# Kernel tuning notes

Measured on AMD Instinct MI355X. Metric: run time of the kernel, lower is better.

Reference implementation:

```python
import jax, jax.numpy as jnp
import numpy as np

WIN = 9  # local window size per spatial dim

def _boxfilter3d(x):
    k = jnp.ones((1, 1, WIN, WIN, WIN), x.dtype) / float(WIN ** 3)
    return jax.lax.conv_general_dilated(
        x, k, window_strides=(1, 1, 1), padding='SAME',
        dimension_numbers=('NCDHW', 'OIDHW', 'NCDHW'))

def setup_inputs() -> dict:
    key = jax.random.key(0)
    k1, k2 = jax.random.split(key)
    shape = (2, 1, 160, 192, 160)
    y_true = jax.random.uniform(k1, shape, dtype=jnp.float32)
    y_pred = jax.random.uniform(k2, shape, dtype=jnp.float32)
    return {"y_true": y_true, "y_pred": y_pred}

def reference(y_true, y_pred):
    Ii, Ji = y_true, y_pred
    mu1 = _boxfilter3d(Ii)
    mu2 = _boxfilter3d(Ji)
    sigma1_sq = _boxfilter3d(Ii * Ii) - mu1 * mu1
    sigma2_sq = _boxfilter3d(Ji * Ji) - mu2 * mu2
    sigma12 = _boxfilter3d(Ii * Ji) - mu1 * mu2
    cc = (sigma12 * sigma12) / (sigma1_sq * sigma2_sq + 1e-5)
    return -jnp.mean(cc)
```

## Files before the change

### kernel.cpp

```cpp
#include <hip/hip_runtime.h>

#define DD 160
#define HH 192
#define WW 160
#define HWs (HH * WW)
#define NTOT 9830400.0f
#define DOUT 20
#define NIT  28
#define NBLK 960

#define SDS 11
#define SDC (24 * SDS + 1)
#define SDP (5 * SDC)
#define HSS 11
#define HSC (16 * HSS + 1)
#define HSP (5 * HSC)

typedef float    v4 __attribute__((ext_vector_type(4)));
typedef _Float16 h4 __attribute__((ext_vector_type(4)));

__device__ __forceinline__ void block_sync_lds() {
    __builtin_amdgcn_s_waitcnt(0xc07f);
    __builtin_amdgcn_s_barrier();
}
__device__ __forceinline__ v4 up(h4 x) { return __builtin_convertvector(x, v4); }
__device__ __forceinline__ h4 dn(v4 x) { return __builtin_convertvector(x, h4); }

__global__ __launch_bounds__(256, 4) void kf(const float* __restrict__ I,
                                             const float* __restrict__ J,
                                             float* __restrict__ partial) {
    __shared__ h4    SDL[2 * SDP];
    __shared__ h4    HSL[2 * HSP];
    __shared__ float red[256];

    const int tid = threadIdx.x;
    const int bx = blockIdx.x, by = blockIdx.y, b = blockIdx.z;
    const int w0 = (bx % 5) * 32, h0 = (bx / 5) * 16;
    const int d0 = by * DOUT;
    const int bid = bx + 60 * (by + 8 * b);

    const int rt = tid ^ ((bx & 1) << 7);

    const bool p1 = rt < 240;
    const int r = rt / 10, g = rt % 10;
    const int gh = h0 - 4 + r, gw = w0 - 4 + g * 4;
    const bool colOK = p1 && gh >= 0 && gh < HH && gw >= 0 && gw < WW;
    const size_t colOff = (size_t)gh * WW + gw;
    const float* Ib = I + (size_t)b * DD * HWs + colOff;
    const float* Jb = J + (size_t)b * DD * HWs + colOff;
    h4* const sdw = &SDL[r * SDS + g];

    const bool p2 = rt < 100;
    const int g2 = rt % 10, ch2 = (rt / 10) % 5, hh0 = (rt / 50) * 8;
    const int sdrOff = ch2 * SDC + hh0 * SDS + g2;
    const int hswOff = ch2 * HSC + hh0 * HSS + g2;

    const bool p3 = rt >= 128;
    const int q3 = rt & 127;
    const int hh = q3 >> 3, sg = q3 & 7;
    const int hsrOff = hh * HSS + sg;

    v4 sd0 = 0.f, sd1 = 0.f, sd2 = 0.f, sd3 = 0.f, sd4 = 0.f;
    h4 fI[9], fJ[9];
#pragma unroll
    for (int u = 0; u < 9; ++u) { fI[u] = (h4)(_Float16)0; fJ[u] = (h4)(_Float16)0; }
    v4 pLI = 0.f, pLJ = 0.f;
    float acc = 0.f;
    const float inv = 1.0f / 729.0f;

    {
        const int si = d0 - 4;
        if (colOK && si >= 0) {
            pLI = *(const v4*)(Ib + (size_t)si * HWs);
            pLJ = *(const v4*)(Jb + (size_t)si * HWs);
        }
    }

    for (int tb = 0; tb < 36; tb += 9) {
#pragma unroll
        for (int u = 0; u < 9; ++u) {
            const int t = tb + u;
            if (t < NIT + 2) {
                if (t < NIT && p1) {
                    h4 cI = dn(pLI), cJ = dn(pLJ);
                    v4 aI = up(cI), aJ = up(cJ);
                    v4 dI = aI, dJv = aJ;
                    v4 dII = aI * aI, dJJ = aJ * aJ, dIJ = aI * aJ;
                    if (t >= 9) {
                        v4 bI = up(fI[u]), bJ = up(fJ[u]);
                        dI -= bI; dJv -= bJ;
                        dII -= bI * bI; dJJ -= bJ * bJ; dIJ -= bI * bJ;
                    }
                    fI[u] = cI; fJ[u] = cJ;
                    sd0 += dI; sd1 += dJv; sd2 += dII; sd3 += dJJ; sd4 += dIJ;
                    h4* const sdq = sdw + (t & 1) * SDP;
                    sdq[0]       = dn(sd0);
                    sdq[SDC]     = dn(sd1);
                    sdq[2 * SDC] = dn(sd2);
                    sdq[3 * SDC] = dn(sd3);
                    sdq[4 * SDC] = dn(sd4);
                    pLI = 0.f; pLJ = 0.f;
                    const int sn = d0 - 3 + t;
                    if (t + 1 < NIT && colOK && sn >= 0 && sn < DD) {
                        pLI = *(const v4*)(Ib + (size_t)sn * HWs);
                        pLJ = *(const v4*)(Jb + (size_t)sn * HWs);
                    }
                }

                if (t >= 1 && t <= NIT && p2) {
                    const int par = (t - 1) & 1;
                    const h4* const sdr = &SDL[par * SDP + sdrOff];
                    h4* const hsw = &HSL[par * HSP + hswOff];
                    h4 s = sdr[0];
#pragma unroll
                    for (int k = 1; k < 9; ++k) s += sdr[k * SDS];
                    hsw[0] = s;
#pragma unroll
                    for (int j = 1; j < 8; ++j) {
                        s += sdr[(j + 8) * SDS] - sdr[(j - 1) * SDS];
                        hsw[j * HSS] = s;
                    }
                }

                if (t >= 10 && p3) {
                    const h4* const hsr = &HSL[(t & 1) * HSP + hsrOff];
                    float w[5][4];
#pragma unroll
                    for (int c = 0; c < 5; ++c) {
                        v4 fa = up(hsr[c * HSC]);
                        v4 fb = up(hsr[c * HSC + 1]);
                        v4 fc = up(hsr[c * HSC + 2]);
                        float s = fa[0] + fa[1] + fa[2] + fa[3] +
                                  fb[0] + fb[1] + fb[2] + fb[3] + fc[0];
                        w[c][0] = s;
                        s += fc[1] - fa[0]; w[c][1] = s;
                        s += fc[2] - fa[1]; w[c][2] = s;
                        s += fc[3] - fa[2]; w[c][3] = s;
                    }
#pragma unroll
                    for (int e = 0; e < 4; ++e) {
                        float mu1 = w[0][e] * inv, mu2 = w[1][e] * inv;
                        float g1  = fmaf(-mu1, mu1, w[2][e] * inv);
                        float g2v = fmaf(-mu2, mu2, w[3][e] * inv);
                        float g12 = fmaf(-mu1, mu2, w[4][e] * inv);
                        acc += __fdividef(g12 * g12, fmaf(g1, g2v, 1e-5f));
                    }
                }

                block_sync_lds();
            }
        }
    }

    red[tid] = acc;
    __syncthreads();
    if (tid < 128) red[tid] += red[tid + 128];
    __syncthreads();
    if (tid < 64) {
        float a = red[tid] + red[tid + 64];
#pragma unroll
        for (int off = 32; off > 0; off >>= 1) a += __shfl_down(a, off);
        if (tid == 0) partial[bid] = a;
    }
}

__global__ void k3_final(const float* __restrict__ partial,
                         float* __restrict__ out) {
    __shared__ float r[1024];
    const int i = threadIdx.x;
    r[i] = (i < NBLK) ? partial[i] : 0.f;
    __syncthreads();
    for (int off = 512; off > 0; off >>= 1) {
        if (i < off) r[i] += r[i + off];
        __syncthreads();
    }
    if (i == 0) out[0] = -r[0] * (1.0f / NTOT);
}

extern "C" void kernel_launch(void* const* d_in, const int* in_sizes, int n_in,
                              void* d_out, int out_size, void* d_ws, size_t ws_size,
                              hipStream_t stream) {
    (void)in_sizes; (void)n_in; (void)out_size; (void)ws_size;
    const float* I = (const float*)d_in[0];
    const float* J = (const float*)d_in[1];
    float* out     = (float*)d_out;
    float* partial = (float*)d_ws;

    dim3 grid(60, 8, 2);
    kf<<<grid, 256, 0, stream>>>(I, J, partial);
    k3_final<<<1, 1024, 0, stream>>>(partial, out);
}
```

Baseline: 151.5 us.

## Interleave channel layout in LDS, double-prefetch loads, and reuse D-sum reads

Rearranges the D-sum LDS buffer so that each column's five channels are stored together, which lets four channels go out as two 16-byte stores instead of five 8-byte stores. Global loads are prefetched two depth slices ahead, alternating between two register buffers, to hide more load latency. The ring buffer becomes 10 entries so the loop unrolls evenly by 10. The H-pass keeps its first seven loaded values in registers instead of reading them from LDS again, and float-to-half conversion now uses packed round-toward-zero cvt_pkrtz. This cuts LDS instruction count and load stalls, at the cost of more registers and slightly different rounding.

```diff
diff --git a/kernel.cpp b/kernel.cpp
--- a/kernel.cpp
+++ b/kernel.cpp
@@ -9,28 +9,33 @@
 #define NIT  28
 #define NBLK 960
 
-#define SDS 11
-#define SDC (24 * SDS + 1)
-#define SDP (5 * SDC)
-#define HSS 11
-#define HSC (16 * HSS + 1)
-#define HSP (5 * HSC)
+#define SDRS 62
+#define SDP  1492
+#define HSRS 10
+#define HSC  162
+#define HSP  810
 
 typedef float    v4 __attribute__((ext_vector_type(4)));
 typedef _Float16 h4 __attribute__((ext_vector_type(4)));
+typedef _Float16 h2 __attribute__((ext_vector_type(2)));
+typedef _Float16 h8 __attribute__((ext_vector_type(8)));
 
 __device__ __forceinline__ void block_sync_lds() {
     __builtin_amdgcn_s_waitcnt(0xc07f);
     __builtin_amdgcn_s_barrier();
 }
 __device__ __forceinline__ v4 up(h4 x) { return __builtin_convertvector(x, v4); }
-__device__ __forceinline__ h4 dn(v4 x) { return __builtin_convertvector(x, h4); }
+__device__ __forceinline__ h4 dnp(v4 x) {
+    h2 a = __builtin_bit_cast(h2, __builtin_amdgcn_cvt_pkrtz(x[0], x[1]));
+    h2 b = __builtin_bit_cast(h2, __builtin_amdgcn_cvt_pkrtz(x[2], x[3]));
+    return __builtin_shufflevector(a, b, 0, 1, 2, 3);
+}
 
 __global__ __launch_bounds__(256, 4) void kf(const float* __restrict__ I,
                                              const float* __restrict__ J,
                                              float* __restrict__ partial) {
-    __shared__ h4    SDL[2 * SDP];
-    __shared__ h4    HSL[2 * HSP];
+    __shared__ __align__(16) h4 SDL[2 * SDP];
+    __shared__ __align__(16) h4 HSL[2 * HSP];
     __shared__ float red[256];
 
     const int tid = threadIdx.x;
@@ -48,107 +53,123 @@
     const size_t colOff = (size_t)gh * WW + gw;
     const float* Ib = I + (size_t)b * DD * HWs + colOff;
     const float* Jb = J + (size_t)b * DD * HWs + colOff;
-    h4* const sdw = &SDL[r * SDS + g];
+    const int sdwOff = r * SDRS + (r >> 3) * 2 + 6 * g;
 
     const bool p2 = rt < 100;
     const int g2 = rt % 10, ch2 = (rt / 10) % 5, hh0 = (rt / 50) * 8;
-    const int sdrOff = ch2 * SDC + hh0 * SDS + g2;
-    const int hswOff = ch2 * HSC + hh0 * HSS + g2;
+    const int sdrOff = hh0 * SDRS + (hh0 >> 3) * 2 + 6 * g2 +
+                       (ch2 == 4 ? 4 + (g2 & 1) : ch2);
+    const int hswOff = ch2 * HSC + hh0 * HSRS + g2;
 
     const bool p3 = rt >= 128;
     const int q3 = rt & 127;
     const int hh = q3 >> 3, sg = q3 & 7;
-    const int hsrOff = hh * HSS + sg;
+    const int hsrOff = hh * HSRS + sg;
 
     v4 sd0 = 0.f, sd1 = 0.f, sd2 = 0.f, sd3 = 0.f, sd4 = 0.f;
-    h4 fI[9], fJ[9];
-#pragma unroll
-    for (int u = 0; u < 9; ++u) { fI[u] = (h4)(_Float16)0; fJ[u] = (h4)(_Float16)0; }
-    v4 pLI = 0.f, pLJ = 0.f;
+    h4 fI[10], fJ[10];
+#pragma unroll
+    for (int uu = 0; uu < 10; ++uu) { fI[uu] = (h4)(_Float16)0; fJ[uu] = (h4)(_Float16)0; }
+    v4 pAI = 0.f, pAJ = 0.f, pBI = 0.f, pBJ = 0.f;
     float acc = 0.f;
     const float inv = 1.0f / 729.0f;
 
     {
-        const int si = d0 - 4;
-        if (colOK && si >= 0) {
-            pLI = *(const v4*)(Ib + (size_t)si * HWs);
-            pLJ = *(const v4*)(Jb + (size_t)si * HWs);
+        const int s0 = d0 - 4;
+        if (colOK && s0 >= 0) {
+            pAI = *(const v4*)(Ib + (size_t)s0 * HWs);
+            pAJ = *(const v4*)(Jb + (size_t)s0 * HWs);
         }
-    }
-
-    for (int tb = 0; tb < 36; tb += 9) {
-#pragma unroll
-        for (int u = 0; u < 9; ++u) {
+        const int s1 = d0 - 3;
+        if (colOK && s1 >= 0) {
+            pBI = *(const v4*)(Ib + (size_t)s1 * HWs);
+            pBJ = *(const v4*)(Jb + (size_t)s1 * HWs);
+        }
+    }
+
+    for (int tb = 0; tb < 30; tb += 10) {
+#pragma unroll
+        for (int u = 0; u < 10; ++u) {
             const int t = tb + u;
-            if (t < NIT + 2) {
-                if (t < NIT && p1) {
-                    h4 cI = dn(pLI), cJ = dn(pLJ);
-                    v4 aI = up(cI), aJ = up(cJ);
-                    v4 dI = aI, dJv = aJ;
-                    v4 dII = aI * aI, dJJ = aJ * aJ, dIJ = aI * aJ;
-                    if (t >= 9) {
-                        v4 bI = up(fI[u]), bJ = up(fJ[u]);
-                        dI -= bI; dJv -= bJ;
-                        dII -= bI * bI; dJJ -= bJ * bJ; dIJ -= bI * bJ;
-                    }
-                    fI[u] = cI; fJ[u] = cJ;
-                    sd0 += dI; sd1 += dJv; sd2 += dII; sd3 += dJJ; sd4 += dIJ;
-                    h4* const sdq = sdw + (t & 1) * SDP;
-                    sdq[0]       = dn(sd0);
-                    sdq[SDC]     = dn(sd1);
-                    sdq[2 * SDC] = dn(sd2);
-                    sdq[3 * SDC] = dn(sd3);
-                    sdq[4 * SDC] = dn(sd4);
-                    pLI = 0.f; pLJ = 0.f;
-                    const int sn = d0 - 3 + t;
-                    if (t + 1 < NIT && colOK && sn >= 0 && sn < DD) {
-                        pLI = *(const v4*)(Ib + (size_t)sn * HWs);
-                        pLJ = *(const v4*)(Jb + (size_t)sn * HWs);
-                    }
-                }
-
-                if (t >= 1 && t <= NIT && p2) {
-                    const int par = (t - 1) & 1;
-                    const h4* const sdr = &SDL[par * SDP + sdrOff];
-                    h4* const hsw = &HSL[par * HSP + hswOff];
-                    h4 s = sdr[0];
-#pragma unroll
-                    for (int k = 1; k < 9; ++k) s += sdr[k * SDS];
-                    hsw[0] = s;
-#pragma unroll
-                    for (int j = 1; j < 8; ++j) {
-                        s += sdr[(j + 8) * SDS] - sdr[(j - 1) * SDS];
-                        hsw[j * HSS] = s;
-                    }
-                }
-
-                if (t >= 10 && p3) {
-                    const h4* const hsr = &HSL[(t & 1) * HSP + hsrOff];
-                    float w[5][4];
-#pragma unroll
-                    for (int c = 0; c < 5; ++c) {
-                        v4 fa = up(hsr[c * HSC]);
-                        v4 fb = up(hsr[c * HSC + 1]);
-                        v4 fc = up(hsr[c * HSC + 2]);
-                        float s = fa[0] + fa[1] + fa[2] + fa[3] +
-                                  fb[0] + fb[1] + fb[2] + fb[3] + fc[0];
-                        w[c][0] = s;
-                        s += fc[1] - fa[0]; w[c][1] = s;
-                        s += fc[2] - fa[1]; w[c][2] = s;
-                        s += fc[3] - fa[2]; w[c][3] = s;
-                    }
-#pragma unroll
-                    for (int e = 0; e < 4; ++e) {
-                        float mu1 = w[0][e] * inv, mu2 = w[1][e] * inv;
-                        float g1  = fmaf(-mu1, mu1, w[2][e] * inv);
-                        float g2v = fmaf(-mu2, mu2, w[3][e] * inv);
-                        float g12 = fmaf(-mu1, mu2, w[4][e] * inv);
-                        acc += __fdividef(g12 * g12, fmaf(g1, g2v, 1e-5f));
-                    }
-                }
-
-                block_sync_lds();
+
+            if (t < NIT && p1) {
+                v4 curI, curJ;
+                if ((u & 1) == 0) { curI = pAI; curJ = pAJ; }
+                else              { curI = pBI; curJ = pBJ; }
+                h4 cI = dnp(curI), cJ = dnp(curJ);
+                v4 aI = up(cI), aJ = up(cJ);
+                v4 dI = aI, dJv = aJ;
+                v4 dII = aI * aI, dJJ = aJ * aJ, dIJ = aI * aJ;
+                if (t >= 9) {
+                    h4 oI = fI[(u + 1) % 10], oJ = fJ[(u + 1) % 10];
+                    v4 bI = up(oI), bJ = up(oJ);
+                    dI -= bI; dJv -= bJ;
+                    dII -= bI * bI; dJJ -= bJ * bJ; dIJ -= bI * bJ;
+                }
+                fI[u] = cI; fJ[u] = cJ;
+                sd0 += dI; sd1 += dJv; sd2 += dII; sd3 += dJJ; sd4 += dIJ;
+                h4* const qb = &SDL[(t & 1) * SDP + sdwOff];
+                h4 c0 = dnp(sd0), c1 = dnp(sd1), c2 = dnp(sd2), c3 = dnp(sd3);
+                *(h8*)qb       = __builtin_shufflevector(c0, c1, 0,1,2,3,4,5,6,7);
+                *(h8*)(qb + 2) = __builtin_shufflevector(c2, c3, 0,1,2,3,4,5,6,7);
+                qb[4 + (g & 1)] = dnp(sd4);
+                v4 nI = 0.f, nJ = 0.f;
+                const int sn = d0 - 2 + t;
+                if (t + 2 < NIT && colOK && sn >= 0 && sn < DD) {
+                    nI = *(const v4*)(Ib + (size_t)sn * HWs);
+                    nJ = *(const v4*)(Jb + (size_t)sn * HWs);
+                }
+                if ((u & 1) == 0) { pAI = nI; pAJ = nJ; }
+                else              { pBI = nI; pBJ = nJ; }
             }
+
+            if (t >= 1 && t <= NIT && p2) {
+                const int par = (t - 1) & 1;
+                const h4* const sdr = &SDL[par * SDP + sdrOff];
+                h4* const hsw = &HSL[par * HSP + hswOff];
+                h4 keep[7];
+                h4 s = sdr[0];
+                keep[0] = s;
+#pragma unroll
+                for (int k = 1; k < 9; ++k) {
+                    h4 v = sdr[k * SDRS + (k >= 8 ? 2 : 0)];
+                    if (k < 7) keep[k] = v;
+                    s += v;
+                }
+                hsw[0] = s;
+#pragma unroll
+                for (int j = 1; j < 8; ++j) {
+                    s += sdr[(j + 8) * SDRS + 2] - keep[j - 1];
+                    hsw[j * HSRS] = s;
+                }
+            }
+
+            if (t >= 10 && p3) {
+                const h4* const hsr = &HSL[(t & 1) * HSP + hsrOff];
+                float w[5][4];
+#pragma unroll
+                for (int c = 0; c < 5; ++c) {
+                    v4 fa = up(hsr[c * HSC]);
+                    v4 fb = up(hsr[c * HSC + 1]);
+                    v4 fc = up(hsr[c * HSC + 2]);
+                    float s = fa[0] + fa[1] + fa[2] + fa[3] +
+                              fb[0] + fb[1] + fb[2] + fb[3] + fc[0];
+                    w[c][0] = s;
+                    s += fc[1] - fa[0]; w[c][1] = s;
+                    s += fc[2] - fa[1]; w[c][2] = s;
+                    s += fc[3] - fa[2]; w[c][3] = s;
+                }
+#pragma unroll
+                for (int e = 0; e < 4; ++e) {
+                    float mu1 = w[0][e] * inv, mu2 = w[1][e] * inv;
+                    float g1  = fmaf(-mu1, mu1, w[2][e] * inv);
+                    float g2v = fmaf(-mu2, mu2, w[3][e] * inv);
+                    float g12 = fmaf(-mu1, mu2, w[4][e] * inv);
+                    acc += __fdividef(g12 * g12, fmaf(g1, g2v, 1e-5f));
+                }
+            }
+
+            block_sync_lds();
         }
     }
 
```

After: 163.0 us. 7.6% more time.
